# Kernel tuning notes

Hardware: AMD Instinct MI355X
Metric: run time of the kernel (lower is better)

Reference implementation:

```python
import jax, jax.numpy as jnp
import numpy as np

NUM_CLASSES = 20
IGNORE_THRESH = 0.5
COORD_SCALE = 1.0
NOOBJ_SCALE = 1.0
OBJ_SCALE = 1.0
CLASS_SCALE = 1.0


def pairwise_iou_xywh(a, b):
    # a: (..., N, 4), b: (..., M, 4), boxes in (cx, cy, w, h) -> IoU (..., N, M)
    ae = a[..., :, None, :]
    be = b[..., None, :, :]
    tl = jnp.maximum(ae[..., :2] - ae[..., 2:] * 0.5, be[..., :2] - be[..., 2:] * 0.5)
    br = jnp.minimum(ae[..., :2] + ae[..., 2:] * 0.5, be[..., :2] + be[..., 2:] * 0.5)
    wh = jnp.maximum(br - tl, 0.0)
    inter = wh[..., 0] * wh[..., 1]
    area_a = ae[..., 2] * ae[..., 3]
    area_b = be[..., 2] * be[..., 3]
    return inter / (area_a + area_b - inter)


def build_targets(outputs, targets, anchors):
    # outputs detached in the torch code -> constants w.r.t. the network output
    o = jax.lax.stop_gradient(outputs)
    B, C, H, W = o.shape
    A = anchors.shape[0]
    HW = H * W
    ch = 5 + NUM_CLASSES
    o5 = o.reshape(B, A, ch, H, W).transpose(0, 1, 3, 4, 2)  # (B, A, H, W, ch)

    x_shift = jnp.arange(W, dtype=o.dtype)            # (W,)
    y_shift = jnp.arange(H, dtype=o.dtype)[:, None]   # (H, 1)
    px = jax.nn.sigmoid(o5[..., 0]) + x_shift
    py = jax.nn.sigmoid(o5[..., 1]) + y_shift
    pw = jnp.exp(o5[..., 2]) * anchors[:, 0][:, None, None]
    ph = jnp.exp(o5[..., 3]) * anchors[:, 1][:, None, None]
    pred = jnp.stack([px, py, pw, ph], -1).transpose(0, 2, 3, 1, 4).reshape(B, HW, A, 4)

    # per-cell anchor boxes, corner-anchored (x_cell, y_cell, aw, ah)
    xs = jnp.broadcast_to(x_shift, (H, W))
    ys = jnp.broadcast_to(jnp.arange(H, dtype=o.dtype)[:, None], (H, W))
    anc = jnp.stack([
        jnp.broadcast_to(xs[:, :, None], (H, W, A)),
        jnp.broadcast_to(ys[:, :, None], (H, W, A)),
        jnp.broadcast_to(anchors[:, 0], (H, W, A)),
        jnp.broadcast_to(anchors[:, 1], (H, W, A))], -1).reshape(HW, A, 4)
    anc_c = anc.at[..., :2].add(0.5)  # center form

    M = targets.shape[1]
    num_obj = jnp.sum(jnp.sum(targets, -1) > 0, axis=1)          # (B,)
    valid = jnp.arange(M)[None, :] < num_obj[:, None]            # (B, M)
    scale = jnp.array([W, H, W, H], o.dtype)
    gt = targets[..., 1:] * scale                                # (B, M, 4) in grid units
    gcls = targets[..., 0]

    # IoU between every pred box and every gt box
    ious = pairwise_iou_xywh(pred.reshape(B, HW * A, 4), gt).reshape(B, HW, A, M)
    ious = jnp.where(valid[:, None, None, :], ious, 0.0)
    max_iou = jnp.max(ious, axis=-1)                             # (B, HW, A)
    has_pos = jnp.any((max_iou > IGNORE_THRESH).reshape(B, -1), axis=1)
    iou_mask = jnp.where(has_pos[:, None, None] & (max_iou >= IGNORE_THRESH), 0.0, 1.0)
    iou_mask = jnp.where((num_obj == 0)[:, None, None], 0.0, iou_mask)

    # anchor/gt overlaps for responsibility assignment
    overlaps = pairwise_iou_xywh(anc_c.reshape(HW * A, 4)[None], gt).reshape(B, HW, A, M)

    cell = (jnp.floor(gt[..., 1]) * W + jnp.floor(gt[..., 0])).astype(jnp.int32)
    cell = jnp.clip(cell, 0, HW - 1)                             # (B, M)
    ov = jnp.take_along_axis(overlaps.transpose(0, 3, 1, 2), cell[:, :, None, None], axis=2)[:, :, 0, :]  # (B, M, A)
    anchor_idx = jnp.argmax(ov, axis=-1)                         # (B, M)
    bidx = jnp.arange(B)[:, None]

    anc_sel = anc[cell, anchor_idx]                              # (B, M, 4)
    delta = jnp.stack([gt[..., 0] - anc_sel[..., 0],
                       gt[..., 1] - anc_sel[..., 1],
                       gt[..., 2] / anc_sel[..., 2],
                       gt[..., 3] / anc_sel[..., 3]], -1)        # (B, M, 4)
    pred_sel = pred[bidx, cell, anchor_idx]                      # (B, M, 4)
    bscale = 2.0 - (pred_sel[..., 2] / W) * (pred_sel[..., 3] / H)
    miou_sel = max_iou[bidx, cell, anchor_idx]                   # (B, M)

    iou_target = jnp.zeros((B, HW, A), o.dtype)
    box_target = jnp.zeros((B, HW, A, 4), o.dtype)
    box_mask = jnp.zeros((B, HW, A), o.dtype)
    box_scale = jnp.zeros((B, HW, A), o.dtype)
    class_target = jnp.zeros((B, HW, A), jnp.int32)
    class_mask = jnp.zeros((B, HW, A), o.dtype)
    b_ar = jnp.arange(B)

    def step(carry, inp):
        it, im, bt, bm, bs, ct, cm = carry
        c, a, v, d, sc, mi, cl = inp
        c_safe = jnp.where(v, c, HW)  # out-of-range -> dropped for padded objects
        it = it.at[b_ar, c_safe, a].set(mi, mode='drop')
        im = im.at[b_ar, c_safe, a].set(2.0, mode='drop')
        bt = bt.at[b_ar, c_safe, a].set(d, mode='drop')
        bm = bm.at[b_ar, c_safe, a].set(1.0, mode='drop')
        bs = bs.at[b_ar, c_safe, a].set(sc, mode='drop')
        ct = ct.at[b_ar, c_safe, a].set(cl.astype(jnp.int32), mode='drop')
        cm = cm.at[b_ar, c_safe, a].set(1.0, mode='drop')
        return (it, im, bt, bm, bs, ct, cm), None

    xs_scan = (cell.T, anchor_idx.T, valid.T, delta.transpose(1, 0, 2),
               bscale.T, miou_sel.T, gcls.T)
    carry, _ = jax.lax.scan(step, (iou_target, iou_mask, box_target, box_mask,
                                   box_scale, class_target, class_mask), xs_scan)
    it, im, bt, bm, bs, ct, cm = carry
    return (it.reshape(-1), im.reshape(-1), bt.reshape(-1, 4), bm.reshape(-1),
            bs.reshape(-1, 1), ct.reshape(-1), cm.reshape(-1))


def yolov2_loss(outputs, targets, anchors):
    it, im, bt, bm, bs, ct, cm = build_targets(outputs, targets, anchors)
    B, C, H, W = outputs.shape
    A = anchors.shape[0]
    ch = 5 + NUM_CLASSES
    o = outputs.reshape(B, A, ch, H, W).transpose(0, 3, 4, 1, 2).reshape(B, H * W * A, ch)
    pred_deltas = jnp.concatenate([jax.nn.sigmoid(o[..., :2]), jnp.exp(o[..., 2:4])], -1).reshape(-1, 4)
    pred_confs = jax.nn.sigmoid(o[..., 4]).reshape(-1)
    pred_probs = o[..., 5:].reshape(-1, NUM_CLASSES)

    s = jnp.sqrt(bs)  # (N, 1); bs is a stop-gradient constant
    box_loss = jnp.sum(bm[:, None] * ((pred_deltas - bt) * s) ** 2)
    obj_iou_loss = jnp.sum(jnp.where(im == 2.0, (pred_confs - it) ** 2, 0.0))
    noobj_iou_loss = jnp.sum(jnp.where(im == 1.0, (pred_confs - it) ** 2, 0.0))
    logp = jax.nn.log_softmax(pred_probs, axis=-1)
    ce = -jnp.take_along_axis(logp, ct[:, None], axis=1)[:, 0]
    class_loss = jnp.sum(cm * ce)
    loss = (COORD_SCALE * box_loss + OBJ_SCALE * obj_iou_loss +
            NOOBJ_SCALE * noobj_iou_loss + CLASS_SCALE * class_loss)
    return loss / B


def setup_inputs() -> dict:
    key = jax.random.key(0)
    k1, k2, k3, k4, k5 = jax.random.split(key, 5)
    B, H, W, A, M = 128, 26, 26, 5, 64
    outputs = jax.random.normal(k1, (B, A * (5 + NUM_CLASSES), H, W), jnp.float32) * 0.5
    cls = jax.random.randint(k2, (B, M, 1), 0, NUM_CLASSES).astype(jnp.float32)
    xy = jax.random.uniform(k3, (B, M, 2), minval=0.05, maxval=0.95)
    wh = jax.random.uniform(k4, (B, M, 2), minval=0.05, maxval=0.5)
    targets = jnp.concatenate([cls, xy, wh], -1)  # (cls, xc, yc, w, h) normalized
    num_obj = jax.random.randint(k5, (B,), 1, M + 1)
    valid = (jnp.arange(M)[None, :] < num_obj[:, None]).astype(jnp.float32)
    targets = targets * valid[:, :, None]  # zero-pad invalid rows (matches gt_num_objs logic)
    anchors = jnp.array([[1.3221, 1.73145], [3.19275, 4.00944], [5.05587, 8.09892],
                         [9.47112, 4.84053], [11.2364, 10.0071]], jnp.float32)
    return {"outputs": outputs, "targets": targets, "anchors": anchors}


def reference(outputs, targets, anchors):
    return yolov2_loss(outputs, targets, anchors)
```

## Files before the change

### kernel.cpp

```cpp
#include <hip/hip_runtime.h>
#include <math.h>

#define NCLS 20
#define B_N 128
#define A_N 5
#define H_N 26
#define W_N 26
#define HW_N (H_N * W_N)
#define M_N 64
#define CH_N (5 + NCLS)
#define HALF_LOC (HW_N / 2)
#define HALF_T (HALF_LOC / 2)
#define BLK_T 192
#define WAVES_PB 3
#define WIN_BLKS B_N
#define NOOBJ_BLKS (B_N * A_N * 2)
#define SLOTS (NOOBJ_BLKS * WAVES_PB)
#define SLOTS_PER_B (A_N * 2 * WAVES_PB)

#define SENT 1.0e18f

__device__ __forceinline__ float fastrcp(float x) { return __builtin_amdgcn_rcpf(x); }
__device__ __forceinline__ float sigmoidf_(float x) { return fastrcp(1.0f + __expf(-x)); }

__global__ __launch_bounds__(BLK_T) void main_kernel(
    const float* __restrict__ outputs, const float* __restrict__ targets,
    const float* __restrict__ anchors,
    float* __restrict__ A_part, float* __restrict__ H_part,
    int* __restrict__ any_part,
    float* __restrict__ Gb, float* __restrict__ Asub, float* __restrict__ Hsub,
    int* __restrict__ nobjArr) {
    int blk = blockIdx.x;
    bool winnerBlk = (blk < WIN_BLKS);
    int tid = threadIdx.x;
    if (winnerBlk && tid >= M_N) return;
    int w = tid >> 6, lane = tid & 63;
    int nb = blk - WIN_BLKS;
    int plane = nb >> 1, half = nb & 1;
    int b = winnerBlk ? blk : (plane / A_N);
    int a = winnerBlk ? 0 : (plane % A_N);

    __shared__ float4 sg4[WAVES_PB * M_N];
    __shared__ int owner[HW_N * A_N];

    const float* trow = targets + ((size_t)b * M_N + lane) * 5;
    float tc = trow[0], tx = trow[1], ty = trow[2], tw = trow[3], th = trow[4];

    float2 O0, O1, O2, O3, O4;
    int hw0 = 0;
    bool act = false;
    if (!winnerBlk) {
        act = (tid < HALF_T);
        if (act) {
            hw0 = half * HALF_LOC + tid * 2;
            const float* op = outputs +
                ((size_t)b * (A_N * CH_N) + (size_t)a * CH_N) * HW_N + hw0;
            O0 = *(const float2*)(op + 0 * HW_N);
            O1 = *(const float2*)(op + 1 * HW_N);
            O2 = *(const float2*)(op + 2 * HW_N);
            O3 = *(const float2*)(op + 3 * HW_N);
            O4 = *(const float2*)(op + 4 * HW_N);
        }
    }

    bool valid = (tc + tx + ty + tw + th) > 0.0f;
    unsigned long long mask = __ballot(valid);
    int nobj = __popcll(mask);
    int nobj8 = (nobj + 7) & ~7;
    float gx = tx * (float)W_N, gy = ty * (float)H_N;
    float gw = tw * (float)W_N, gh = th * (float)H_N;
    float4 g4 = valid ? make_float4(gx - gw * 0.5f, gy - gh * 0.5f,
                                    gx + gw * 0.5f, gy + gh * 0.5f)
                      : make_float4(SENT, SENT, SENT, SENT);
    float4* myg = sg4 + w * M_N;
    myg[lane] = g4;
    __threadfence_block();

    if (winnerBlk) {
        float G = 0.0f, c2A = 0.0f, c2H = 0.0f;
        int m = lane;
        int cell = (int)floorf(gy) * W_N + (int)floorf(gx);
        cell = min(max(cell, 0), HW_N - 1);
        int ccx = cell % W_N, ccy = cell / W_N;
        float best = -1.0f;
        int ai = 0; float aw = 1.0f, ah = 1.0f;
        float ga = gw * gh;
        #pragma unroll
        for (int aa = 0; aa < A_N; ++aa) {
            float anw = anchors[2 * aa], anh = anchors[2 * aa + 1];
            float atlx = (float)ccx + 0.5f - anw * 0.5f;
            float atly = (float)ccy + 0.5f - anh * 0.5f;
            float ix = fminf(atlx + anw, g4.z) - fmaxf(atlx, g4.x);
            float iy = fminf(atly + anh, g4.w) - fmaxf(atly, g4.y);
            float inter = fmaxf(ix, 0.0f) * fmaxf(iy, 0.0f);
            float ov = inter * fastrcp(anw * anh + ga - inter);
            if (ov > best) { best = ov; ai = aa; aw = anw; ah = anh; }
        }
        int mykey = cell * A_N + ai;

        if (valid) owner[mykey] = 0;
        __threadfence_block();
        if (valid) atomicMax(&owner[mykey], m);
        __threadfence_block();
        bool winner = valid && (owner[mykey] == m);

        if (winner) {
            size_t obase = ((size_t)b * (A_N * CH_N) + (size_t)ai * CH_N) * HW_N + cell;
            float o0 = outputs[obase + 0 * HW_N];
            float o1 = outputs[obase + 1 * HW_N];
            float o2 = outputs[obase + 2 * HW_N];
            float o3 = outputs[obase + 3 * HW_N];
            float o4 = outputs[obase + 4 * HW_N];
            float sx = sigmoidf_(o0), sy = sigmoidf_(o1);
            float ew = __expf(o2), eh = __expf(o3);
            float conf = sigmoidf_(o4);
            float px = sx + (float)ccx, py = sy + (float)ccy;
            float pw = ew * aw, ph = eh * ah;
            float ptlx = px - pw * 0.5f, ptly = py - ph * 0.5f;
            float pbrx = px + pw * 0.5f, pbry = py + ph * 0.5f;
            float pa = pw * ph;

            float mi = 0.0f, maxdW = -1e30f;
            #pragma unroll 4
            for (int mm = 0; mm < nobj8; ++mm) {
                float4 g = myg[mm];
                float gaM = (g.z - g.x) * (g.w - g.y);
                float ix = fminf(pbrx, g.z) - fmaxf(ptlx, g.x);
                float iy = fminf(pbry, g.w) - fmaxf(ptly, g.y);
                float inter = fmaxf(ix, 0.0f) * fmaxf(iy, 0.0f);
                mi = fmaxf(mi, inter * fastrcp(pa + gaM - inter));
                maxdW = fmaxf(maxdW, fmaf(3.0f, inter, -(pa + gaM)));
            }

            float dcf = conf - mi;
            G = dcf * dcf;
            float bs = 2.0f - (pw / (float)W_N) * (ph / (float)H_N);
            float e0 = sx - (gx - (float)ccx);
            float e1 = sy - (gy - (float)ccy);
            float e2 = ew - gw / aw;
            float e3 = eh - gh / ah;
            G += bs * (e0 * e0 + e1 * e1 + e2 * e2 + e3 * e3);

            int cls = (int)tc;
            float mx = -1e30f, tv = 0.0f, logits[NCLS];
            #pragma unroll
            for (int c = 0; c < NCLS; ++c) {
                logits[c] = outputs[obase + (size_t)(5 + c) * HW_N];
                mx = fmaxf(mx, logits[c]);
            }
            float se = 0.0f;
            #pragma unroll
            for (int c = 0; c < NCLS; ++c) {
                se += __expf(logits[c] - mx);
                if (c == cls) tv = logits[c];
            }
            G += (mx + __logf(se)) - tv;

            c2A = conf * conf;
            c2H = (maxdW >= 0.0f) ? c2A : 0.0f;
        }
        #pragma unroll
        for (int off = 32; off > 0; off >>= 1) {
            G   += __shfl_down(G, off);
            c2A += __shfl_down(c2A, off);
            c2H += __shfl_down(c2H, off);
        }
        if (lane == 0) {
            Gb[b] = G; Asub[b] = c2A; Hsub[b] = c2H; nobjArr[b] = nobj;
        }
    } else {
        float locA = 0.0f, locH = 0.0f;
        bool any = false;
        if (act) {
            int wy = hw0 / W_N;
            int wx = hw0 - wy * W_N;
            float aw = anchors[2 * a], ah = anchors[2 * a + 1];

            float sx0 = sigmoidf_(O0.x), sx1 = sigmoidf_(O0.y);
            float sy0 = sigmoidf_(O1.x), sy1 = sigmoidf_(O1.y);
            float pw0 = __expf(O2.x) * aw, pw1 = __expf(O2.y) * aw;
            float ph0 = __expf(O3.x) * ah, ph1 = __expf(O3.y) * ah;
            float px0 = sx0 + (float)wx, px1 = sx1 + (float)(wx + 1);
            float py0 = sy0 + (float)wy, py1 = sy1 + (float)wy;

            float ptlx0 = px0 - pw0 * 0.5f, ptly0 = py0 - ph0 * 0.5f;
            float pbrx0 = px0 + pw0 * 0.5f, pbry0 = py0 + ph0 * 0.5f;
            float ptlx1 = px1 - pw1 * 0.5f, ptly1 = py1 - ph1 * 0.5f;
            float pbrx1 = px1 + pw1 * 0.5f, pbry1 = py1 + ph1 * 0.5f;
            float pa0 = pw0 * ph0, pa1 = pw1 * ph1;

            float maxd0 = -1e30f, maxd1 = -1e30f;
            for (int m = 0; m < nobj8; m += 8) {
                #pragma unroll
                for (int k = 0; k < 8; ++k) {
                    float4 g = myg[m + k];
                    float ga = (g.z - g.x) * (g.w - g.y);
                    float ix0 = fminf(pbrx0, g.z) - fmaxf(ptlx0, g.x);
                    float iy0 = fminf(pbry0, g.w) - fmaxf(ptly0, g.y);
                    float in0 = fmaxf(ix0, 0.0f) * fmaxf(iy0, 0.0f);
                    maxd0 = fmaxf(maxd0, fmaf(3.0f, in0, -(pa0 + ga)));
                    float ix1 = fminf(pbrx1, g.z) - fmaxf(ptlx1, g.x);
                    float iy1 = fminf(pbry1, g.w) - fmaxf(ptly1, g.y);
                    float in1 = fmaxf(ix1, 0.0f) * fmaxf(iy1, 0.0f);
                    maxd1 = fmaxf(maxd1, fmaf(3.0f, in1, -(pa1 + ga)));
                }
            }
            float conf0 = sigmoidf_(O4.x), conf1 = sigmoidf_(O4.y);
            float c20 = conf0 * conf0, c21 = conf1 * conf1;
            locA = c20 + c21;
            locH = (maxd0 >= 0.0f ? c20 : 0.0f) + (maxd1 >= 0.0f ? c21 : 0.0f);
            any = (maxd0 > 0.0f) || (maxd1 > 0.0f);
        }

        int wany = __any(any) ? 1 : 0;
        #pragma unroll
        for (int off = 32; off > 0; off >>= 1) {
            locA += __shfl_down(locA, off);
            locH += __shfl_down(locH, off);
        }
        if (lane == 0) {
            int slot = nb * WAVES_PB + w;
            A_part[slot] = locA;
            H_part[slot] = locH;
            any_part[slot] = wany;
        }
    }
}

__global__ __launch_bounds__(128) void finish_kernel(
    const float* __restrict__ A_part, const float* __restrict__ H_part,
    const int* __restrict__ any_part,
    const float* __restrict__ Gb, const float* __restrict__ Asub,
    const float* __restrict__ Hsub, const int* __restrict__ nobjArr,
    float* __restrict__ out) {
    int t = threadIdx.x;
    float A = -Asub[t], Hs = -Hsub[t];
    int any = 0;
    #pragma unroll
    for (int j = 0; j < SLOTS_PER_B; ++j) {
        A += A_part[t * SLOTS_PER_B + j];
        Hs += H_part[t * SLOTS_PER_B + j];
        any |= any_part[t * SLOTS_PER_B + j];
    }
    float noobj = (nobjArr[t] > 0) ? (A - (any ? Hs : 0.0f)) : 0.0f;
    float v = Gb[t] + noobj;
    #pragma unroll
    for (int off = 32; off > 0; off >>= 1) v += __shfl_down(v, off);
    __shared__ float r[2];
    if ((t & 63) == 0) r[t >> 6] = v;
    __syncthreads();
    if (t == 0) out[0] = (r[0] + r[1]) / (float)B_N;
}

extern "C" void kernel_launch(void* const* d_in, const int* in_sizes, int n_in,
                              void* d_out, int out_size, void* d_ws, size_t ws_size,
                              hipStream_t stream) {
    const float* outputs = (const float*)d_in[0];
    const float* targets = (const float*)d_in[1];
    const float* anchors = (const float*)d_in[2];
    float* out = (float*)d_out;

    char* ws = (char*)d_ws;
    size_t off = 0;
    float* A_part = (float*)(ws + off); off += 4 * (size_t)SLOTS;
    float* H_part = (float*)(ws + off); off += 4 * (size_t)SLOTS;
    int* any_part = (int*)(ws + off);   off += 4 * (size_t)SLOTS;
    float* Gb = (float*)(ws + off);     off += 4 * B_N;
    float* Asub = (float*)(ws + off);   off += 4 * B_N;
    float* Hsub = (float*)(ws + off);   off += 4 * B_N;
    int* nobjArr = (int*)(ws + off);    off += 4 * B_N;

    main_kernel<<<WIN_BLKS + NOOBJ_BLKS, BLK_T, 0, stream>>>(
        outputs, targets, anchors,
        A_part, H_part, any_part, Gb, Asub, Hsub, nobjArr);

    finish_kernel<<<1, 128, 0, stream>>>(A_part, H_part, any_part,
                                         Gb, Asub, Hsub, nobjArr, out);
}
```

Baseline: 20.60 us.

## Broadcast GT boxes via readlane, one cell per thread, block-level partial reduction

Replaces the shared-memory float4 table of ground-truth boxes with wavefront readlane broadcasts of register values, and precomputes GT areas. The no-object path moves from two cells per thread in 192-thread blocks to one cell per thread in 384-thread blocks. Partial sums are reduced within each block before being written, which shrinks the finish kernel's input. Winner selection now uses a linear scan over keys in shared memory instead of atomicMax, removing the LDS traffic and atomics at the cost of a scalar-dependent loop and less per-thread ILP.

```diff
diff --git a/kernel.cpp b/kernel.cpp
--- a/kernel.cpp
+++ b/kernel.cpp
@@ -10,20 +10,20 @@
 #define M_N 64
 #define CH_N (5 + NCLS)
 #define HALF_LOC (HW_N / 2)
-#define HALF_T (HALF_LOC / 2)
-#define BLK_T 192
-#define WAVES_PB 3
+#define BLK_T 384
+#define WAVES_PB 6
 #define WIN_BLKS B_N
 #define NOOBJ_BLKS (B_N * A_N * 2)
-#define SLOTS (NOOBJ_BLKS * WAVES_PB)
-#define SLOTS_PER_B (A_N * 2 * WAVES_PB)
-
+#define SLOTS_PER_B (A_N * 2)
 #define SENT 1.0e18f
 
 __device__ __forceinline__ float fastrcp(float x) { return __builtin_amdgcn_rcpf(x); }
 __device__ __forceinline__ float sigmoidf_(float x) { return fastrcp(1.0f + __expf(-x)); }
-
-__global__ __launch_bounds__(BLK_T) void main_kernel(
+__device__ __forceinline__ float rdlane(float v, int m) {
+    return __int_as_float(__builtin_amdgcn_readlane(__float_as_int(v), m));
+}
+
+__global__ __launch_bounds__(BLK_T, 8) void main_kernel(
     const float* __restrict__ outputs, const float* __restrict__ targets,
     const float* __restrict__ anchors,
     float* __restrict__ A_part, float* __restrict__ H_part,
@@ -34,47 +34,46 @@
     bool winnerBlk = (blk < WIN_BLKS);
     int tid = threadIdx.x;
     if (winnerBlk && tid >= M_N) return;
-    int w = tid >> 6, lane = tid & 63;
-    int nb = blk - WIN_BLKS;
-    int plane = nb >> 1, half = nb & 1;
-    int b = winnerBlk ? blk : (plane / A_N);
-    int a = winnerBlk ? 0 : (plane % A_N);
-
-    __shared__ float4 sg4[WAVES_PB * M_N];
-    __shared__ int owner[HW_N * A_N];
+    int lane = tid & 63;
+
+    int b, a, half;
+    if (winnerBlk) { b = blk; a = 0; half = 0; }
+    else {
+        int nb = blk - WIN_BLKS;
+        int plane = nb >> 1; half = nb & 1;
+        b = plane / A_N; a = plane % A_N;
+    }
+
+    __shared__ int skey[M_N];
+    __shared__ float rA[WAVES_PB], rH[WAVES_PB];
+    __shared__ int rAny[WAVES_PB];
 
     const float* trow = targets + ((size_t)b * M_N + lane) * 5;
     float tc = trow[0], tx = trow[1], ty = trow[2], tw = trow[3], th = trow[4];
 
-    float2 O0, O1, O2, O3, O4;
-    int hw0 = 0;
-    bool act = false;
+    float O0 = 0, O1 = 0, O2 = 0, O3 = 0, O4 = 0;
+    int hw = 0; bool act = false;
     if (!winnerBlk) {
-        act = (tid < HALF_T);
-        if (act) {
-            hw0 = half * HALF_LOC + tid * 2;
-            const float* op = outputs +
-                ((size_t)b * (A_N * CH_N) + (size_t)a * CH_N) * HW_N + hw0;
-            O0 = *(const float2*)(op + 0 * HW_N);
-            O1 = *(const float2*)(op + 1 * HW_N);
-            O2 = *(const float2*)(op + 2 * HW_N);
-            O3 = *(const float2*)(op + 3 * HW_N);
-            O4 = *(const float2*)(op + 4 * HW_N);
-        }
+        act = (tid < HALF_LOC);
+        hw = half * HALF_LOC + (act ? tid : 0);
+        const float* op = outputs +
+            ((size_t)b * (A_N * CH_N) + (size_t)a * CH_N) * HW_N + hw;
+        O0 = op[0 * HW_N]; O1 = op[1 * HW_N]; O2 = op[2 * HW_N];
+        O3 = op[3 * HW_N]; O4 = op[4 * HW_N];
     }
 
     bool valid = (tc + tx + ty + tw + th) > 0.0f;
     unsigned long long mask = __ballot(valid);
     int nobj = __popcll(mask);
-    int nobj8 = (nobj + 7) & ~7;
     float gx = tx * (float)W_N, gy = ty * (float)H_N;
     float gw = tw * (float)W_N, gh = th * (float)H_N;
-    float4 g4 = valid ? make_float4(gx - gw * 0.5f, gy - gh * 0.5f,
-                                    gx + gw * 0.5f, gy + gh * 0.5f)
-                      : make_float4(SENT, SENT, SENT, SENT);
-    float4* myg = sg4 + w * M_N;
-    myg[lane] = g4;
-    __threadfence_block();
+    float g0, g1, g2, g3, ga;
+    if (valid) {
+        g0 = gx - gw * 0.5f; g1 = gy - gh * 0.5f;
+        g2 = gx + gw * 0.5f; g3 = gy + gh * 0.5f; ga = gw * gh;
+    } else {
+        g0 = SENT; g1 = SENT; g2 = SENT; g3 = SENT; ga = 0.0f;
+    }
 
     if (winnerBlk) {
         float G = 0.0f, c2A = 0.0f, c2H = 0.0f;
@@ -84,25 +83,26 @@
         int ccx = cell % W_N, ccy = cell / W_N;
         float best = -1.0f;
         int ai = 0; float aw = 1.0f, ah = 1.0f;
-        float ga = gw * gh;
         #pragma unroll
         for (int aa = 0; aa < A_N; ++aa) {
             float anw = anchors[2 * aa], anh = anchors[2 * aa + 1];
             float atlx = (float)ccx + 0.5f - anw * 0.5f;
             float atly = (float)ccy + 0.5f - anh * 0.5f;
-            float ix = fminf(atlx + anw, g4.z) - fmaxf(atlx, g4.x);
-            float iy = fminf(atly + anh, g4.w) - fmaxf(atly, g4.y);
+            float ix = fminf(atlx + anw, g2) - fmaxf(atlx, g0);
+            float iy = fminf(atly + anh, g3) - fmaxf(atly, g1);
             float inter = fmaxf(ix, 0.0f) * fmaxf(iy, 0.0f);
             float ov = inter * fastrcp(anw * anh + ga - inter);
             if (ov > best) { best = ov; ai = aa; aw = anw; ah = anh; }
         }
         int mykey = cell * A_N + ai;
-
-        if (valid) owner[mykey] = 0;
-        __threadfence_block();
-        if (valid) atomicMax(&owner[mykey], m);
-        __threadfence_block();
-        bool winner = valid && (owner[mykey] == m);
+        skey[m] = valid ? mykey : (-1 - m);
+        __builtin_amdgcn_s_waitcnt(0);
+
+        bool winner = valid;
+        if (valid) {
+            for (int mm = m + 1; mm < M_N; ++mm)
+                if (skey[mm] == mykey) winner = false;
+        }
 
         if (winner) {
             size_t obase = ((size_t)b * (A_N * CH_N) + (size_t)ai * CH_N) * HW_N + cell;
@@ -116,20 +116,20 @@
             float conf = sigmoidf_(o4);
             float px = sx + (float)ccx, py = sy + (float)ccy;
             float pw = ew * aw, ph = eh * ah;
-            float ptlx = px - pw * 0.5f, ptly = py - ph * 0.5f;
-            float pbrx = px + pw * 0.5f, pbry = py + ph * 0.5f;
+            float tlx = px - pw * 0.5f, tly = py - ph * 0.5f;
+            float brx = px + pw * 0.5f, bry = py + ph * 0.5f;
             float pa = pw * ph;
 
             float mi = 0.0f, maxdW = -1e30f;
-            #pragma unroll 4
-            for (int mm = 0; mm < nobj8; ++mm) {
-                float4 g = myg[mm];
-                float gaM = (g.z - g.x) * (g.w - g.y);
-                float ix = fminf(pbrx, g.z) - fmaxf(ptlx, g.x);
-                float iy = fminf(pbry, g.w) - fmaxf(ptly, g.y);
-                float inter = fmaxf(ix, 0.0f) * fmaxf(iy, 0.0f);
-                mi = fmaxf(mi, inter * fastrcp(pa + gaM - inter));
-                maxdW = fmaxf(maxdW, fmaf(3.0f, inter, -(pa + gaM)));
+            for (int mm = 0; mm < nobj; ++mm) {
+                float q0 = rdlane(g0, mm), q1 = rdlane(g1, mm);
+                float q2 = rdlane(g2, mm), q3 = rdlane(g3, mm);
+                float qa = rdlane(ga, mm);
+                float ix = fminf(brx, q2) - fmaxf(tlx, q0);
+                float iy = fminf(bry, q3) - fmaxf(tly, q1);
+                float in = fmaxf(ix, 0.0f) * fmaxf(iy, 0.0f);
+                mi = fmaxf(mi, in * fastrcp(pa + qa - in));
+                maxdW = fmaxf(maxdW, fmaf(3.0f, in, -(pa + qa)));
             }
 
             float dcf = conf - mi;
@@ -142,17 +142,16 @@
             G += bs * (e0 * e0 + e1 * e1 + e2 * e2 + e3 * e3);
 
             int cls = (int)tc;
-            float mx = -1e30f, tv = 0.0f, logits[NCLS];
+            float mx = -1e30f;
+            #pragma unroll
+            for (int c = 0; c < NCLS; ++c)
+                mx = fmaxf(mx, outputs[obase + (size_t)(5 + c) * HW_N]);
+            float se = 0.0f, tv = 0.0f;
             #pragma unroll
             for (int c = 0; c < NCLS; ++c) {
-                logits[c] = outputs[obase + (size_t)(5 + c) * HW_N];
-                mx = fmaxf(mx, logits[c]);
-            }
-            float se = 0.0f;
-            #pragma unroll
-            for (int c = 0; c < NCLS; ++c) {
-                se += __expf(logits[c] - mx);
-                if (c == cls) tv = logits[c];
+                float v = outputs[obase + (size_t)(5 + c) * HW_N];
+                se += __expf(v - mx);
+                if (c == cls) tv = v;
             }
             G += (mx + __logf(se)) - tv;
 
@@ -169,47 +168,38 @@
             Gb[b] = G; Asub[b] = c2A; Hsub[b] = c2H; nobjArr[b] = nobj;
         }
     } else {
-        float locA = 0.0f, locH = 0.0f;
-        bool any = false;
+        unsigned wy = (unsigned)hw / (unsigned)W_N;
+        unsigned wx = (unsigned)hw - wy * (unsigned)W_N;
+        float aw = anchors[2 * a], ah = anchors[2 * a + 1];
+        float sx = sigmoidf_(O0), sy = sigmoidf_(O1);
+        float pw = __expf(O2) * aw, ph = __expf(O3) * ah;
+        float px = sx + (float)wx, py = sy + (float)wy;
+        float tlx = px - pw * 0.5f, tly = py - ph * 0.5f;
+        float brx = px + pw * 0.5f, bry = py + ph * 0.5f;
+        float pa = pw * ph;
+
+        float maxd = -1e30f;
+        int nobj4 = (nobj + 3) & ~3;
+        for (int m = 0; m < nobj4; m += 4) {
+            #pragma unroll
+            for (int k = 0; k < 4; ++k) {
+                int mm = m + k;
+                float q0 = rdlane(g0, mm), q1 = rdlane(g1, mm);
+                float q2 = rdlane(g2, mm), q3 = rdlane(g3, mm);
+                float qa = rdlane(ga, mm);
+                float ix = fminf(brx, q2) - fmaxf(tlx, q0);
+                float iy = fminf(bry, q3) - fmaxf(tly, q1);
+                float in = fmaxf(ix, 0.0f) * fmaxf(iy, 0.0f);
+                maxd = fmaxf(maxd, fmaf(3.0f, in, -(pa + qa)));
+            }
+        }
+        float locA = 0.0f, locH = 0.0f; bool any = false;
         if (act) {
-            int wy = hw0 / W_N;
-            int wx = hw0 - wy * W_N;
-            float aw = anchors[2 * a], ah = anchors[2 * a + 1];
-
-            float sx0 = sigmoidf_(O0.x), sx1 = sigmoidf_(O0.y);
-            float sy0 = sigmoidf_(O1.x), sy1 = sigmoidf_(O1.y);
-            float pw0 = __expf(O2.x) * aw, pw1 = __expf(O2.y) * aw;
-            float ph0 = __expf(O3.x) * ah, ph1 = __expf(O3.y) * ah;
-            float px0 = sx0 + (float)wx, px1 = sx1 + (float)(wx + 1);
-            float py0 = sy0 + (float)wy, py1 = sy1 + (float)wy;
-
-            float ptlx0 = px0 - pw0 * 0.5f, ptly0 = py0 - ph0 * 0.5f;
-            float pbrx0 = px0 + pw0 * 0.5f, pbry0 = py0 + ph0 * 0.5f;
-            float ptlx1 = px1 - pw1 * 0.5f, ptly1 = py1 - ph1 * 0.5f;
-            float pbrx1 = px1 + pw1 * 0.5f, pbry1 = py1 + ph1 * 0.5f;
-            float pa0 = pw0 * ph0, pa1 = pw1 * ph1;
-
-            float maxd0 = -1e30f, maxd1 = -1e30f;
-            for (int m = 0; m < nobj8; m += 8) {
-                #pragma unroll
-                for (int k = 0; k < 8; ++k) {
-                    float4 g = myg[m + k];
-                    float ga = (g.z - g.x) * (g.w - g.y);
-                    float ix0 = fminf(pbrx0, g.z) - fmaxf(ptlx0, g.x);
-                    float iy0 = fminf(pbry0, g.w) - fmaxf(ptly0, g.y);
-                    float in0 = fmaxf(ix0, 0.0f) * fmaxf(iy0, 0.0f);
-                    maxd0 = fmaxf(maxd0, fmaf(3.0f, in0, -(pa0 + ga)));
-                    float ix1 = fminf(pbrx1, g.z) - fmaxf(ptlx1, g.x);
-                    float iy1 = fminf(pbry1, g.w) - fmaxf(ptly1, g.y);
-                    float in1 = fmaxf(ix1, 0.0f) * fmaxf(iy1, 0.0f);
-                    maxd1 = fmaxf(maxd1, fmaf(3.0f, in1, -(pa1 + ga)));
-                }
-            }
-            float conf0 = sigmoidf_(O4.x), conf1 = sigmoidf_(O4.y);
-            float c20 = conf0 * conf0, c21 = conf1 * conf1;
-            locA = c20 + c21;
-            locH = (maxd0 >= 0.0f ? c20 : 0.0f) + (maxd1 >= 0.0f ? c21 : 0.0f);
-            any = (maxd0 > 0.0f) || (maxd1 > 0.0f);
+            float conf = sigmoidf_(O4);
+            float c2 = conf * conf;
+            locA = c2;
+            locH = (maxd >= 0.0f) ? c2 : 0.0f;
+            any = (maxd > 0.0f);
         }
 
         int wany = __any(any) ? 1 : 0;
@@ -218,11 +208,17 @@
             locA += __shfl_down(locA, off);
             locH += __shfl_down(locH, off);
         }
-        if (lane == 0) {
-            int slot = nb * WAVES_PB + w;
-            A_part[slot] = locA;
-            H_part[slot] = locH;
-            any_part[slot] = wany;
+        int w = tid >> 6;
+        if (lane == 0) { rA[w] = locA; rH[w] = locH; rAny[w] = wany; }
+        __syncthreads();
+        if (tid == 0) {
+            float A = 0.0f, Hs = 0.0f; int anyT = 0;
+            #pragma unroll
+            for (int j = 0; j < WAVES_PB; ++j) {
+                A += rA[j]; Hs += rH[j]; anyT |= rAny[j];
+            }
+            int nb = blk - WIN_BLKS;
+            A_part[nb] = A; H_part[nb] = Hs; any_part[nb] = anyT;
         }
     }
 }
@@ -262,9 +258,9 @@
 
     char* ws = (char*)d_ws;
     size_t off = 0;
-    float* A_part = (float*)(ws + off); off += 4 * (size_t)SLOTS;
-    float* H_part = (float*)(ws + off); off += 4 * (size_t)SLOTS;
-    int* any_part = (int*)(ws + off);   off += 4 * (size_t)SLOTS;
+    float* A_part = (float*)(ws + off); off += 4 * (size_t)NOOBJ_BLKS;
+    float* H_part = (float*)(ws + off); off += 4 * (size_t)NOOBJ_BLKS;
+    int* any_part = (int*)(ws + off);   off += 4 * (size_t)NOOBJ_BLKS;
     float* Gb = (float*)(ws + off);     off += 4 * B_N;
     float* Asub = (float*)(ws + off);   off += 4 * B_N;
     float* Hsub = (float*)(ws + off);   off += 4 * B_N;
```

Measured after the change: 31.82 us. +54.5%, slower.

## Share GT boxes across waves, skip non-overlapping rows, use shuffle winner dedup

Applied to the files above, without the earlier changes.

Targets are loaded once per block by the first wave into shared memory, not separately by every wave, and are consumed after a block barrier. The no-object loop now iterates exactly nobj boxes and uses a wave-wide y-overlap test to skip the x/area work for boxes no lane overlaps. The predicted area is moved out of the loop comparison. Winner deduplication uses a lane-shuffle scan instead of shared-memory atomics, and per-wave partials are reduced in shared memory so each block writes one slot. This adds block barriers and a divergent-branch check in exchange for less redundant loading and arithmetic.

```diff
diff --git a/kernel.cpp b/kernel.cpp
--- a/kernel.cpp
+++ b/kernel.cpp
@@ -12,12 +12,9 @@
 #define HALF_LOC (HW_N / 2)
 #define HALF_T (HALF_LOC / 2)
 #define BLK_T 192
-#define WAVES_PB 3
 #define WIN_BLKS B_N
 #define NOOBJ_BLKS (B_N * A_N * 2)
-#define SLOTS (NOOBJ_BLKS * WAVES_PB)
-#define SLOTS_PER_B (A_N * 2 * WAVES_PB)
-
+#define SLOTS_PER_B (A_N * 2)
 #define SENT 1.0e18f
 
 __device__ __forceinline__ float fastrcp(float x) { return __builtin_amdgcn_rcpf(x); }
@@ -33,22 +30,24 @@
     int blk = blockIdx.x;
     bool winnerBlk = (blk < WIN_BLKS);
     int tid = threadIdx.x;
-    if (winnerBlk && tid >= M_N) return;
-    int w = tid >> 6, lane = tid & 63;
-    int nb = blk - WIN_BLKS;
-    int plane = nb >> 1, half = nb & 1;
-    int b = winnerBlk ? blk : (plane / A_N);
-    int a = winnerBlk ? 0 : (plane % A_N);
-
-    __shared__ float4 sg4[WAVES_PB * M_N];
-    __shared__ int owner[HW_N * A_N];
-
-    const float* trow = targets + ((size_t)b * M_N + lane) * 5;
-    float tc = trow[0], tx = trow[1], ty = trow[2], tw = trow[3], th = trow[4];
-
+    int lane = tid & 63;
+
+    int b, a, half;
+    if (winnerBlk) { b = blk; a = 0; half = 0; }
+    else {
+        int nb = blk - WIN_BLKS;
+        int plane = nb >> 1; half = nb & 1;
+        b = plane / A_N; a = plane % A_N;
+    }
+
+    __shared__ float4 sg4[M_N];
+    __shared__ int snobj;
+    __shared__ float rA[3], rH[3];
+    __shared__ int rAny[3];
+
+    bool act = false;
     float2 O0, O1, O2, O3, O4;
     int hw0 = 0;
-    bool act = false;
     if (!winnerBlk) {
         act = (tid < HALF_T);
         if (act) {
@@ -63,28 +62,33 @@
         }
     }
 
-    bool valid = (tc + tx + ty + tw + th) > 0.0f;
-    unsigned long long mask = __ballot(valid);
-    int nobj = __popcll(mask);
-    int nobj8 = (nobj + 7) & ~7;
-    float gx = tx * (float)W_N, gy = ty * (float)H_N;
-    float gw = tw * (float)W_N, gh = th * (float)H_N;
-    float4 g4 = valid ? make_float4(gx - gw * 0.5f, gy - gh * 0.5f,
-                                    gx + gw * 0.5f, gy + gh * 0.5f)
-                      : make_float4(SENT, SENT, SENT, SENT);
-    float4* myg = sg4 + w * M_N;
-    myg[lane] = g4;
-    __threadfence_block();
+    float tc = 0, gx = 0, gy = 0, gw = 0, gh = 0;
+    bool valid = false;
+    if (tid < M_N) {
+        const float* trow = targets + ((size_t)b * M_N + tid) * 5;
+        tc = trow[0];
+        float tx = trow[1], ty = trow[2], tw = trow[3], th = trow[4];
+        valid = (tc + tx + ty + tw + th) > 0.0f;
+        unsigned long long mask = __ballot(valid);
+        if (tid == 0) snobj = __popcll(mask);
+        gx = tx * (float)W_N; gy = ty * (float)H_N;
+        gw = tw * (float)W_N; gh = th * (float)H_N;
+        sg4[tid] = make_float4(gx - gw * 0.5f, gy - gh * 0.5f,
+                               gx + gw * 0.5f, gy + gh * 0.5f);
+    }
+    __syncthreads();
+    int nobj = snobj;
 
     if (winnerBlk) {
+        if (tid >= M_N) return;
         float G = 0.0f, c2A = 0.0f, c2H = 0.0f;
-        int m = lane;
+        float4 g4 = sg4[lane];
+        float ga = gw * gh;
         int cell = (int)floorf(gy) * W_N + (int)floorf(gx);
         cell = min(max(cell, 0), HW_N - 1);
         int ccx = cell % W_N, ccy = cell / W_N;
         float best = -1.0f;
         int ai = 0; float aw = 1.0f, ah = 1.0f;
-        float ga = gw * gh;
         #pragma unroll
         for (int aa = 0; aa < A_N; ++aa) {
             float anw = anchors[2 * aa], anh = anchors[2 * aa + 1];
@@ -96,13 +100,12 @@
             float ov = inter * fastrcp(anw * anh + ga - inter);
             if (ov > best) { best = ov; ai = aa; aw = anw; ah = anh; }
         }
-        int mykey = cell * A_N + ai;
-
-        if (valid) owner[mykey] = 0;
-        __threadfence_block();
-        if (valid) atomicMax(&owner[mykey], m);
-        __threadfence_block();
-        bool winner = valid && (owner[mykey] == m);
+        int mykey = valid ? (cell * A_N + ai) : (-1 - lane);
+        bool winner = valid;
+        for (int d = 1; d < M_N; ++d) {
+            int ok = __shfl_down(mykey, d);
+            if ((lane + d) < M_N && ok == mykey) winner = false;
+        }
 
         if (winner) {
             size_t obase = ((size_t)b * (A_N * CH_N) + (size_t)ai * CH_N) * HW_N + cell;
@@ -116,20 +119,19 @@
             float conf = sigmoidf_(o4);
             float px = sx + (float)ccx, py = sy + (float)ccy;
             float pw = ew * aw, ph = eh * ah;
-            float ptlx = px - pw * 0.5f, ptly = py - ph * 0.5f;
-            float pbrx = px + pw * 0.5f, pbry = py + ph * 0.5f;
+            float tlx = px - pw * 0.5f, tly = py - ph * 0.5f;
+            float brx = px + pw * 0.5f, bry = py + ph * 0.5f;
             float pa = pw * ph;
 
             float mi = 0.0f, maxdW = -1e30f;
-            #pragma unroll 4
-            for (int mm = 0; mm < nobj8; ++mm) {
-                float4 g = myg[mm];
+            for (int mm = 0; mm < nobj; ++mm) {
+                float4 g = sg4[mm];
                 float gaM = (g.z - g.x) * (g.w - g.y);
-                float ix = fminf(pbrx, g.z) - fmaxf(ptlx, g.x);
-                float iy = fminf(pbry, g.w) - fmaxf(ptly, g.y);
-                float inter = fmaxf(ix, 0.0f) * fmaxf(iy, 0.0f);
-                mi = fmaxf(mi, inter * fastrcp(pa + gaM - inter));
-                maxdW = fmaxf(maxdW, fmaf(3.0f, inter, -(pa + gaM)));
+                float ix = fminf(brx, g.z) - fmaxf(tlx, g.x);
+                float iy = fminf(bry, g.w) - fmaxf(tly, g.y);
+                float in = fmaxf(ix, 0.0f) * fmaxf(iy, 0.0f);
+                mi = fmaxf(mi, in * fastrcp(pa + gaM - in));
+                maxdW = fmaxf(maxdW, fmaf(3.0f, in, -(pa + gaM)));
             }
 
             float dcf = conf - mi;
@@ -169,47 +171,52 @@
             Gb[b] = G; Asub[b] = c2A; Hsub[b] = c2H; nobjArr[b] = nobj;
         }
     } else {
-        float locA = 0.0f, locH = 0.0f;
-        bool any = false;
+        float tlx0, tly0, brx0, bry0, pa0, tlx1, tly1, brx1, bry1, pa1;
         if (act) {
             int wy = hw0 / W_N;
             int wx = hw0 - wy * W_N;
             float aw = anchors[2 * a], ah = anchors[2 * a + 1];
-
             float sx0 = sigmoidf_(O0.x), sx1 = sigmoidf_(O0.y);
             float sy0 = sigmoidf_(O1.x), sy1 = sigmoidf_(O1.y);
             float pw0 = __expf(O2.x) * aw, pw1 = __expf(O2.y) * aw;
             float ph0 = __expf(O3.x) * ah, ph1 = __expf(O3.y) * ah;
             float px0 = sx0 + (float)wx, px1 = sx1 + (float)(wx + 1);
             float py0 = sy0 + (float)wy, py1 = sy1 + (float)wy;
-
-            float ptlx0 = px0 - pw0 * 0.5f, ptly0 = py0 - ph0 * 0.5f;
-            float pbrx0 = px0 + pw0 * 0.5f, pbry0 = py0 + ph0 * 0.5f;
-            float ptlx1 = px1 - pw1 * 0.5f, ptly1 = py1 - ph1 * 0.5f;
-            float pbrx1 = px1 + pw1 * 0.5f, pbry1 = py1 + ph1 * 0.5f;
-            float pa0 = pw0 * ph0, pa1 = pw1 * ph1;
-
-            float maxd0 = -1e30f, maxd1 = -1e30f;
-            for (int m = 0; m < nobj8; m += 8) {
-                #pragma unroll
-                for (int k = 0; k < 8; ++k) {
-                    float4 g = myg[m + k];
-                    float ga = (g.z - g.x) * (g.w - g.y);
-                    float ix0 = fminf(pbrx0, g.z) - fmaxf(ptlx0, g.x);
-                    float iy0 = fminf(pbry0, g.w) - fmaxf(ptly0, g.y);
-                    float in0 = fmaxf(ix0, 0.0f) * fmaxf(iy0, 0.0f);
-                    maxd0 = fmaxf(maxd0, fmaf(3.0f, in0, -(pa0 + ga)));
-                    float ix1 = fminf(pbrx1, g.z) - fmaxf(ptlx1, g.x);
-                    float iy1 = fminf(pbry1, g.w) - fmaxf(ptly1, g.y);
-                    float in1 = fmaxf(ix1, 0.0f) * fmaxf(iy1, 0.0f);
-                    maxd1 = fmaxf(maxd1, fmaf(3.0f, in1, -(pa1 + ga)));
-                }
-            }
+            tlx0 = px0 - pw0 * 0.5f; tly0 = py0 - ph0 * 0.5f;
+            brx0 = px0 + pw0 * 0.5f; bry0 = py0 + ph0 * 0.5f;
+            tlx1 = px1 - pw1 * 0.5f; tly1 = py1 - ph1 * 0.5f;
+            brx1 = px1 + pw1 * 0.5f; bry1 = py1 + ph1 * 0.5f;
+            pa0 = pw0 * ph0; pa1 = pw1 * ph1;
+        } else {
+            tlx0 = tlx1 = SENT; tly0 = tly1 = SENT;
+            brx0 = brx1 = -SENT; bry0 = bry1 = -SENT;
+            pa0 = pa1 = SENT;
+        }
+
+        float maxs0 = -1e30f, maxs1 = -1e30f;
+        for (int m = 0; m < nobj; ++m) {
+            float4 g = sg4[m];
+            float iy0 = fminf(bry0, g.w) - fmaxf(tly0, g.y);
+            float iy1 = fminf(bry1, g.w) - fmaxf(tly1, g.y);
+            if (__any(fmaxf(iy0, iy1) > 0.0f)) {
+                float ga = (g.z - g.x) * (g.w - g.y);
+                float ix0 = fminf(brx0, g.z) - fmaxf(tlx0, g.x);
+                float in0 = fmaxf(ix0, 0.0f) * fmaxf(iy0, 0.0f);
+                maxs0 = fmaxf(maxs0, fmaf(3.0f, in0, -ga));
+                float ix1 = fminf(brx1, g.z) - fmaxf(tlx1, g.x);
+                float in1 = fmaxf(ix1, 0.0f) * fmaxf(iy1, 0.0f);
+                maxs1 = fmaxf(maxs1, fmaf(3.0f, in1, -ga));
+            }
+        }
+
+        float locA = 0.0f, locH = 0.0f;
+        bool any = false;
+        if (act) {
             float conf0 = sigmoidf_(O4.x), conf1 = sigmoidf_(O4.y);
             float c20 = conf0 * conf0, c21 = conf1 * conf1;
             locA = c20 + c21;
-            locH = (maxd0 >= 0.0f ? c20 : 0.0f) + (maxd1 >= 0.0f ? c21 : 0.0f);
-            any = (maxd0 > 0.0f) || (maxd1 > 0.0f);
+            locH = (maxs0 >= pa0 ? c20 : 0.0f) + (maxs1 >= pa1 ? c21 : 0.0f);
+            any = (maxs0 > pa0) || (maxs1 > pa1);
         }
 
         int wany = __any(any) ? 1 : 0;
@@ -218,11 +225,14 @@
             locA += __shfl_down(locA, off);
             locH += __shfl_down(locH, off);
         }
-        if (lane == 0) {
-            int slot = nb * WAVES_PB + w;
-            A_part[slot] = locA;
-            H_part[slot] = locH;
-            any_part[slot] = wany;
+        int w = tid >> 6;
+        if (lane == 0) { rA[w] = locA; rH[w] = locH; rAny[w] = wany; }
+        __syncthreads();
+        if (tid == 0) {
+            int nb = blk - WIN_BLKS;
+            A_part[nb] = rA[0] + rA[1] + rA[2];
+            H_part[nb] = rH[0] + rH[1] + rH[2];
+            any_part[nb] = rAny[0] | rAny[1] | rAny[2];
         }
     }
 }
@@ -262,9 +272,9 @@
 
     char* ws = (char*)d_ws;
     size_t off = 0;
-    float* A_part = (float*)(ws + off); off += 4 * (size_t)SLOTS;
-    float* H_part = (float*)(ws + off); off += 4 * (size_t)SLOTS;
-    int* any_part = (int*)(ws + off);   off += 4 * (size_t)SLOTS;
+    float* A_part = (float*)(ws + off); off += 4 * (size_t)NOOBJ_BLKS;
+    float* H_part = (float*)(ws + off); off += 4 * (size_t)NOOBJ_BLKS;
+    int* any_part = (int*)(ws + off);   off += 4 * (size_t)NOOBJ_BLKS;
     float* Gb = (float*)(ws + off);     off += 4 * B_N;
     float* Asub = (float*)(ws + off);   off += 4 * B_N;
     float* Hsub = (float*)(ws + off);   off += 4 * B_N;
```

Result: slower. 22.64 us (+9.9%).
